# Kernel optimization log

Measured on AMD Instinct MI355X. Metric: run time of the kernel, lower is better.

The kernel has to match this reference:

```python
import jax, jax.numpy as jnp
import numpy as np

B, T, C, H = 4, 2048, 1024, 128  # batch, block_size, n_embds, head_size


def setup_inputs() -> dict:
    key = jax.random.key(0)
    k1, k2, k3, k4 = jax.random.split(key, 4)
    x = jax.random.normal(k1, (B, T, C), dtype=jnp.float32)
    # Linear(n_embds, head_size, bias=False) weights, stored as [C, H] so q = x @ Wq
    s = C ** -0.5
    Wq = jax.random.normal(k2, (C, H), dtype=jnp.float32) * s
    Wk = jax.random.normal(k3, (C, H), dtype=jnp.float32) * s
    Wv = jax.random.normal(k4, (C, H), dtype=jnp.float32) * s
    return {"x": x, "Wq": Wq, "Wk": Wk, "Wv": Wv}


def reference(x, Wq, Wk, Wv):
    # q, k, v projections (no bias)
    q = x @ Wq  # [B, T, H]
    k = x @ Wk  # [B, T, H]
    v = x @ Wv  # [B, T, H]
    scale = q.shape[-1] ** -0.5
    wei = jnp.einsum('btd,bsd->bts', q, k) * scale  # [B, T, T]
    # causal mask: positions where tril == 0 (upper triangle) get -inf
    t = wei.shape[1]
    causal = jnp.tril(jnp.ones((t, t), dtype=bool))
    wei = jnp.where(causal, wei, -jnp.inf)
    # NOTE: source uses F.softmax(wei, dim=1) -> normalize over the QUERY axis
    wei = jax.nn.softmax(wei, axis=1)
    out = wei @ v  # [B, T, H]
    return out
```

## Files before the change

### kernel.cpp

```cpp
#include <hip/hip_runtime.h>
#include <math.h>

#define B_ 4
#define T_ 2048
#define C_ 1024
#define H_ 128
#define RCHUNK 128
#define NCHUNK (T_ / RCHUNK)

typedef unsigned short u16;
typedef unsigned int   u32;
typedef short short8  __attribute__((ext_vector_type(8)));
typedef short short4v __attribute__((ext_vector_type(4)));
typedef float floatx4 __attribute__((ext_vector_type(4)));

__device__ __forceinline__ u16 f2bf(float f) {
    union { float f; u32 u; } v; v.f = f;
    return (u16)((v.u + 0x7fffu + ((v.u >> 16) & 1u)) >> 16);
}
__device__ __forceinline__ float bf2f(u16 h) {
    union { u32 u; float f; } v; v.u = ((u32)h) << 16;
    return v.f;
}

__global__ __launch_bounds__(256) void convert_x_kernel(
    const float* __restrict__ x, u16* __restrict__ xb)
{
    const size_t i = ((size_t)blockIdx.x * 256 + threadIdx.x) * 8;
    float4 a = *(const float4*)&x[i];
    float4 b = *(const float4*)&x[i + 4];
    short8 o;
    o[0]=(short)f2bf(a.x); o[1]=(short)f2bf(a.y); o[2]=(short)f2bf(a.z); o[3]=(short)f2bf(a.w);
    o[4]=(short)f2bf(b.x); o[5]=(short)f2bf(b.y); o[6]=(short)f2bf(b.z); o[7]=(short)f2bf(b.w);
    *(short8*)&xb[i] = o;
}

__global__ __launch_bounds__(256) void convert_w_kernel(
    const float* __restrict__ Wq, const float* __restrict__ Wk,
    const float* __restrict__ Wv, u16* __restrict__ Wt)
{
    const int k0 = blockIdx.x * 64, n0 = blockIdx.y * 64, widx = blockIdx.z;
    const float* W = (widx == 0) ? Wq : (widx == 1) ? Wk : Wv;

    __shared__ float ts[64][68];
    for (int i = threadIdx.x; i < 64 * 16; i += 256) {
        int r = i >> 4, c4 = i & 15;
        float4 v = *(const float4*)&W[(size_t)(k0 + r) * H_ + n0 + c4 * 4];
        ts[r][c4 * 4 + 0] = v.x; ts[r][c4 * 4 + 1] = v.y;
        ts[r][c4 * 4 + 2] = v.z; ts[r][c4 * 4 + 3] = v.w;
    }
    __syncthreads();
    for (int i = threadIdx.x; i < 64 * 16; i += 256) {
        int n = i >> 4, k4 = i & 15;
        short4v o;
        #pragma unroll
        for (int j = 0; j < 4; ++j) o[j] = (short)f2bf(ts[k4 * 4 + j][n]);
        *(short4v*)&Wt[(size_t)widx * H_ * C_ + (size_t)(n0 + n) * C_ + k0 + k4 * 4] = o;
    }
}

__global__ __launch_bounds__(256) void qkv_gemm_kernel(
    const u16* __restrict__ xb, const u16* __restrict__ Wt,
    u16* __restrict__ Qb, u16* __restrict__ Kb, u16* __restrict__ Vt)
{
    const int m0   = blockIdx.x * 64;
    const int widx = blockIdx.y;
    const u16* Wg = Wt + (size_t)widx * H_ * C_;

    __shared__ u16 As[64 * 136];
    __shared__ u16 Bs[128 * 136];

    const int w    = threadIdx.x >> 6;
    const int lane = threadIdx.x & 63;
    const int q    = lane >> 4, r = lane & 15;

    floatx4 acc[8] = {};

    for (int k0 = 0; k0 < C_; k0 += 128) {
        for (int i = threadIdx.x; i < 64 * 16; i += 256) {
            int rr = i >> 4, c = i & 15;
            *(float4*)&As[rr * 136 + c * 8] =
                *(const float4*)&xb[(size_t)(m0 + rr) * C_ + k0 + c * 8];
        }
        for (int i = threadIdx.x; i < 128 * 16; i += 256) {
            int rr = i >> 4, c = i & 15;
            *(float4*)&Bs[rr * 136 + c * 8] =
                *(const float4*)&Wg[(size_t)rr * C_ + k0 + c * 8];
        }
        __syncthreads();

        #pragma unroll
        for (int kk = 0; kk < 4; ++kk) {
            short8 af = *(const short8*)&As[(16 * w + r) * 136 + kk * 32 + q * 8];
            #pragma unroll
            for (int nt = 0; nt < 8; ++nt) {
                short8 bf = *(const short8*)&Bs[(16 * nt + r) * 136 + kk * 32 + q * 8];
                acc[nt] = __builtin_amdgcn_mfma_f32_16x16x32_bf16(af, bf, acc[nt], 0, 0, 0);
            }
        }
        __syncthreads();
    }

    if (widx == 2) {
        const int bb  = m0 / T_;
        const int tt0 = (m0 - bb * T_) + 16 * w + q * 4;
        #pragma unroll
        for (int nt = 0; nt < 8; ++nt) {
            short4v o;
            #pragma unroll
            for (int reg = 0; reg < 4; ++reg) o[reg] = (short)f2bf(acc[nt][reg]);
            *(short4v*)&Vt[((size_t)bb * H_ + 16 * nt + r) * T_ + tt0] = o;
        }
    } else {
        u16* dst = (widx == 0) ? Qb : Kb;
        #pragma unroll
        for (int nt = 0; nt < 8; ++nt)
            #pragma unroll
            for (int reg = 0; reg < 4; ++reg) {
                int mm = m0 + 16 * w + q * 4 + reg;
                int nn = 16 * nt + r;
                dst[(size_t)mm * H_ + nn] = f2bf(acc[nt][reg]);
            }
    }
}

__global__ __launch_bounds__(256) void scores_kernel(
    const u16* __restrict__ Qb, const u16* __restrict__ Kb,
    u16* __restrict__ S, float* __restrict__ pm, float* __restrict__ pl)
{
    const int si = blockIdx.x;
    const int ti = blockIdx.y;
    const int b  = blockIdx.z;
    if (si > 2 * ti + 1) return;
    const int t0 = ti * 128, s0 = si * 64;
    const bool diag = (si >= 2 * ti);

    __shared__ u16 smem[128 * 136 + 64 * 136];
    u16* Qs = smem;
    u16* Ks = smem + 128 * 136;

    const u16* Qg = Qb + ((size_t)b * T_ + t0) * H_;
    const u16* Kg = Kb + ((size_t)b * T_ + s0) * H_;

    for (int i = threadIdx.x; i < 128 * 16; i += 256) {
        int rr = i >> 4, c = i & 15;
        *(float4*)&Qs[rr * 136 + c * 8] = *(const float4*)&Qg[(size_t)rr * H_ + c * 8];
    }
    for (int i = threadIdx.x; i < 64 * 16; i += 256) {
        int rr = i >> 4, c = i & 15;
        *(float4*)&Ks[rr * 136 + c * 8] = *(const float4*)&Kg[(size_t)rr * H_ + c * 8];
    }
    __syncthreads();

    const int w    = threadIdx.x >> 6;
    const int lane = threadIdx.x & 63;
    const int q    = lane >> 4, r = lane & 15;

    floatx4 acc[2][4] = {};
    #pragma unroll
    for (int kk = 0; kk < 4; ++kk) {
        short8 a0 = *(const short8*)&Qs[(32 * w +      r) * 136 + kk * 32 + q * 8];
        short8 a1 = *(const short8*)&Qs[(32 * w + 16 + r) * 136 + kk * 32 + q * 8];
        #pragma unroll
        for (int nt = 0; nt < 4; ++nt) {
            short8 bf = *(const short8*)&Ks[(16 * nt + r) * 136 + kk * 32 + q * 8];
            acc[0][nt] = __builtin_amdgcn_mfma_f32_16x16x32_bf16(a0, bf, acc[0][nt], 0, 0, 0);
            acc[1][nt] = __builtin_amdgcn_mfma_f32_16x16x32_bf16(a1, bf, acc[1][nt], 0, 0, 0);
        }
    }
    __syncthreads();

    u16*   tile = smem;
    float* redm = (float*)(smem + 128 * 72);
    float* redl = redm + 16 * 64;

    const float scale = 0.08838834764831845f;
    #pragma unroll
    for (int nt = 0; nt < 4; ++nt) {
        const int s = s0 + 16 * nt + r;
        float mx = -INFINITY, sm = 0.f;
        #pragma unroll
        for (int mt = 0; mt < 2; ++mt)
            #pragma unroll
            for (int reg = 0; reg < 4; ++reg) {
                const int tl = 32 * w + 16 * mt + q * 4 + reg;
                const float v = acc[mt][nt][reg] * scale;
                tile[tl * 72 + 16 * nt + r] = f2bf(v);
                if (!diag || (t0 + tl) >= s) {
                    float mn = fmaxf(mx, v);
                    sm = sm * __expf(mx - mn) + __expf(v - mn);
                    mx = mn;
                }
            }
        redm[(4 * w + q) * 64 + 16 * nt + r] = mx;
        redl[(4 * w + q) * 64 + 16 * nt + r] = sm;
    }
    __syncthreads();

    if (threadIdx.x < 64) {
        const int c = threadIdx.x;
        float M = -INFINITY;
        #pragma unroll
        for (int g = 0; g < 16; ++g) M = fmaxf(M, redm[g * 64 + c]);
        float L = 0.f;
        #pragma unroll
        for (int g = 0; g < 16; ++g) {
            float lg = redl[g * 64 + c];
            if (lg > 0.f) L += lg * __expf(redm[g * 64 + c] - M);
        }
        const size_t o = ((size_t)b * NCHUNK + ti) * T_ + s0 + c;
        pm[o] = M;
        pl[o] = L;
    }

    u16* Sg = S + ((size_t)b * T_ + t0) * T_ + s0;
    for (int i = threadIdx.x; i < 128 * 8; i += 256) {
        int tl = i >> 3, c8 = i & 7;
        *(float4*)&Sg[(size_t)tl * T_ + c8 * 8] = *(float4*)&tile[tl * 72 + c8 * 8];
    }
}

__global__ __launch_bounds__(256) void stats_reduce_kernel(
    const float* __restrict__ pm, const float* __restrict__ pl,
    float* __restrict__ m, float* __restrict__ linv)
{
    const int idx = blockIdx.x * 256 + threadIdx.x;
    const int b = idx >> 11, s = idx & (T_ - 1);
    const int c0 = s >> 7;

    float M = -INFINITY;
    for (int c = c0; c < NCHUNK; ++c)
        M = fmaxf(M, pm[((size_t)b * NCHUNK + c) * T_ + s]);

    float L = 0.f;
    for (int c = c0; c < NCHUNK; ++c) {
        float mc = pm[((size_t)b * NCHUNK + c) * T_ + s];
        float lc = pl[((size_t)b * NCHUNK + c) * T_ + s];
        if (lc > 0.f) L += lc * __expf(mc - M);
    }
    m[idx]    = M;
    linv[idx] = 1.0f / L;
}

__global__ __launch_bounds__(256) void out_kernel(
    const u16* __restrict__ S, const u16* __restrict__ Vt,
    const float* __restrict__ m, const float* __restrict__ linv,
    float* __restrict__ out)
{
    const int b  = blockIdx.y;
    const int tb = (int)(gridDim.x - 1 - blockIdx.x);
    const int t0 = tb * 16;
    const int nchunks = (t0 + 79) >> 6;

    const int w    = threadIdx.x >> 6;
    const int lane = threadIdx.x & 63;
    const int q    = lane >> 4, r = lane & 15;
    const int t    = t0 + r;

    const u16*   Sb  = S    + ((size_t)b * T_ + t) * T_;
    const float* mB  = m    + (size_t)b * T_;
    const float* lB  = linv + (size_t)b * T_;
    const u16*   VtB = Vt   + (size_t)b * H_ * T_;

    floatx4 acc[8] = {};

    for (int ci = w; ci < nchunks; ci += 4) {
        const int s0 = ci * 64;
        #pragma unroll
        for (int kk = 0; kk < 2; ++kk) {
            const int sb = s0 + kk * 32 + q * 8;
            short8 sraw = *(const short8*)&Sb[sb];
            float mv[8], lv[8];
            *(float4*)&mv[0] = *(const float4*)&mB[sb];
            *(float4*)&mv[4] = *(const float4*)&mB[sb + 4];
            *(float4*)&lv[0] = *(const float4*)&lB[sb];
            *(float4*)&lv[4] = *(const float4*)&lB[sb + 4];

            short8 af;
            #pragma unroll
            for (int j = 0; j < 8; ++j) {
                float wj = 0.f;
                if (sb + j <= t)
                    wj = __expf(bf2f((u16)sraw[j]) - mv[j]) * lv[j];
                af[j] = (short)f2bf(wj);
            }
            #pragma unroll
            for (int nt = 0; nt < 8; ++nt) {
                short8 bf = *(const short8*)&VtB[(size_t)(16 * nt + r) * T_ + sb];
                acc[nt] = __builtin_amdgcn_mfma_f32_16x16x32_bf16(af, bf, acc[nt], 0, 0, 0);
            }
        }
    }

    __shared__ float red[4][16 * 128];
    #pragma unroll
    for (int nt = 0; nt < 8; ++nt)
        #pragma unroll
        for (int reg = 0; reg < 4; ++reg)
            red[w][(q * 4 + reg) * 128 + 16 * nt + r] = acc[nt][reg];
    __syncthreads();

    float* outB = out + ((size_t)b * T_ + t0) * H_;
    for (int i = threadIdx.x; i < 16 * 128; i += 256)
        outB[i] = red[0][i] + red[1][i] + red[2][i] + red[3][i];
}

extern "C" void kernel_launch(void* const* d_in, const int* in_sizes, int n_in,
                              void* d_out, int out_size, void* d_ws, size_t ws_size,
                              hipStream_t stream) {
    const float* x  = (const float*)d_in[0];
    const float* Wq = (const float*)d_in[1];
    const float* Wk = (const float*)d_in[2];
    const float* Wv = (const float*)d_in[3];
    float* out = (float*)d_out;

    u16*   S    = (u16*)d_ws;
    float* m    = (float*)(S + (size_t)B_ * T_ * T_);
    float* linv = m + (size_t)B_ * T_;
    u16*   Wt   = (u16*)(linv + (size_t)B_ * T_);
    u16*   Qb   = Wt + (size_t)3 * H_ * C_;
    u16*   Kb   = Qb + (size_t)B_ * T_ * H_;
    u16*   Vt   = Kb + (size_t)B_ * T_ * H_;
    u16*   xb   = S;

    float* pm = (float*)d_out;
    float* pl = pm + (size_t)B_ * NCHUNK * T_;

    convert_x_kernel  <<<dim3(B_ * T_ * C_ / (256 * 8)), dim3(256), 0, stream>>>(x, xb);
    convert_w_kernel  <<<dim3(C_ / 64, H_ / 64, 3),      dim3(256), 0, stream>>>(Wq, Wk, Wv, Wt);
    qkv_gemm_kernel   <<<dim3(B_ * T_ / 64, 3),          dim3(256), 0, stream>>>(xb, Wt, Qb, Kb, Vt);
    scores_kernel     <<<dim3(32, 16, B_),               dim3(256), 0, stream>>>(Qb, Kb, S, pm, pl);
    stats_reduce_kernel<<<dim3(B_ * T_ / 256),           dim3(256), 0, stream>>>(pm, pl, m, linv);
    out_kernel        <<<dim3(T_ / 16, B_),              dim3(256), 0, stream>>>(S, Vt, m, linv, out);
}
```

Measured before the change: 183.9 us.

## Recompute scores in output kernel instead of materializing S; fuse x conversion into GEMM

The scores kernel no longer writes the full bf16 score matrix to global memory and only produces per-chunk column max/sum statistics. The output kernel recomputes QK^T per 64x64 tile from Q and K in shared memory, applies the column-softmax normalisation, and multiplies by V. This avoids writing and reading the large B*T*T score matrix. Separately, the fp32-to-bf16 conversion of x moves into the QKV GEMM load path, which removes one kernel launch and an intermediate buffer. In exchange QK^T is computed twice, and the output kernel loops serially over up to 32 chunks per block with barriers, using larger tiles and fewer blocks.

```diff
diff --git a/kernel.cpp b/kernel.cpp
--- a/kernel.cpp
+++ b/kernel.cpp
@@ -18,22 +18,6 @@
     union { float f; u32 u; } v; v.f = f;
     return (u16)((v.u + 0x7fffu + ((v.u >> 16) & 1u)) >> 16);
 }
-__device__ __forceinline__ float bf2f(u16 h) {
-    union { u32 u; float f; } v; v.u = ((u32)h) << 16;
-    return v.f;
-}
-
-__global__ __launch_bounds__(256) void convert_x_kernel(
-    const float* __restrict__ x, u16* __restrict__ xb)
-{
-    const size_t i = ((size_t)blockIdx.x * 256 + threadIdx.x) * 8;
-    float4 a = *(const float4*)&x[i];
-    float4 b = *(const float4*)&x[i + 4];
-    short8 o;
-    o[0]=(short)f2bf(a.x); o[1]=(short)f2bf(a.y); o[2]=(short)f2bf(a.z); o[3]=(short)f2bf(a.w);
-    o[4]=(short)f2bf(b.x); o[5]=(short)f2bf(b.y); o[6]=(short)f2bf(b.z); o[7]=(short)f2bf(b.w);
-    *(short8*)&xb[i] = o;
-}
 
 __global__ __launch_bounds__(256) void convert_w_kernel(
     const float* __restrict__ Wq, const float* __restrict__ Wk,
@@ -60,7 +44,7 @@
 }
 
 __global__ __launch_bounds__(256) void qkv_gemm_kernel(
-    const u16* __restrict__ xb, const u16* __restrict__ Wt,
+    const float* __restrict__ x, const u16* __restrict__ Wt,
     u16* __restrict__ Qb, u16* __restrict__ Kb, u16* __restrict__ Vt)
 {
     const int m0   = blockIdx.x * 64;
@@ -79,8 +63,15 @@
     for (int k0 = 0; k0 < C_; k0 += 128) {
         for (int i = threadIdx.x; i < 64 * 16; i += 256) {
             int rr = i >> 4, c = i & 15;
-            *(float4*)&As[rr * 136 + c * 8] =
-                *(const float4*)&xb[(size_t)(m0 + rr) * C_ + k0 + c * 8];
+            const float* xg = &x[(size_t)(m0 + rr) * C_ + k0 + c * 8];
+            float4 a = *(const float4*)xg;
+            float4 b = *(const float4*)(xg + 4);
+            short8 o;
+            o[0]=(short)f2bf(a.x); o[1]=(short)f2bf(a.y);
+            o[2]=(short)f2bf(a.z); o[3]=(short)f2bf(a.w);
+            o[4]=(short)f2bf(b.x); o[5]=(short)f2bf(b.y);
+            o[6]=(short)f2bf(b.z); o[7]=(short)f2bf(b.w);
+            *(short8*)&As[rr * 136 + c * 8] = o;
         }
         for (int i = threadIdx.x; i < 128 * 16; i += 256) {
             int rr = i >> 4, c = i & 15;
@@ -124,9 +115,9 @@
     }
 }
 
-__global__ __launch_bounds__(256) void scores_kernel(
+__global__ __launch_bounds__(256) void stats_kernel(
     const u16* __restrict__ Qb, const u16* __restrict__ Kb,
-    u16* __restrict__ S, float* __restrict__ pm, float* __restrict__ pl)
+    float* __restrict__ pm, float* __restrict__ pl)
 {
     const int si = blockIdx.x;
     const int ti = blockIdx.y;
@@ -170,8 +161,7 @@
     }
     __syncthreads();
 
-    u16*   tile = smem;
-    float* redm = (float*)(smem + 128 * 72);
+    float* redm = (float*)smem;
     float* redl = redm + 16 * 64;
 
     const float scale = 0.08838834764831845f;
@@ -185,7 +175,6 @@
             for (int reg = 0; reg < 4; ++reg) {
                 const int tl = 32 * w + 16 * mt + q * 4 + reg;
                 const float v = acc[mt][nt][reg] * scale;
-                tile[tl * 72 + 16 * nt + r] = f2bf(v);
                 if (!diag || (t0 + tl) >= s) {
                     float mn = fmaxf(mx, v);
                     sm = sm * __expf(mx - mn) + __expf(v - mn);
@@ -212,12 +201,6 @@
         pm[o] = M;
         pl[o] = L;
     }
-
-    u16* Sg = S + ((size_t)b * T_ + t0) * T_ + s0;
-    for (int i = threadIdx.x; i < 128 * 8; i += 256) {
-        int tl = i >> 3, c8 = i & 7;
-        *(float4*)&Sg[(size_t)tl * T_ + c8 * 8] = *(float4*)&tile[tl * 72 + c8 * 8];
-    }
 }
 
 __global__ __launch_bounds__(256) void stats_reduce_kernel(
@@ -243,66 +226,96 @@
 }
 
 __global__ __launch_bounds__(256) void out_kernel(
-    const u16* __restrict__ S, const u16* __restrict__ Vt,
+    const u16* __restrict__ Qb, const u16* __restrict__ Kb,
+    const u16* __restrict__ Vt,
     const float* __restrict__ m, const float* __restrict__ linv,
     float* __restrict__ out)
 {
     const int b  = blockIdx.y;
     const int tb = (int)(gridDim.x - 1 - blockIdx.x);
-    const int t0 = tb * 16;
-    const int nchunks = (t0 + 79) >> 6;
+    const int t0 = tb * 64;
+    const int nch = tb + 1;
+
+    __shared__ u16 Qs[64 * 136];
+    __shared__ u16 Ks[64 * 136];
+    __shared__ u16 Ps[64 * 72];
+    __shared__ float ms[64], ls[64];
 
     const int w    = threadIdx.x >> 6;
     const int lane = threadIdx.x & 63;
     const int q    = lane >> 4, r = lane & 15;
-    const int t    = t0 + r;
-
-    const u16*   Sb  = S    + ((size_t)b * T_ + t) * T_;
+
+    const u16* Qg = Qb + ((size_t)b * T_ + t0) * H_;
+    for (int i = threadIdx.x; i < 64 * 16; i += 256) {
+        int rr = i >> 4, c = i & 15;
+        *(float4*)&Qs[rr * 136 + c * 8] = *(const float4*)&Qg[(size_t)rr * H_ + c * 8];
+    }
+
     const float* mB  = m    + (size_t)b * T_;
     const float* lB  = linv + (size_t)b * T_;
     const u16*   VtB = Vt   + (size_t)b * H_ * T_;
-
-    floatx4 acc[8] = {};
-
-    for (int ci = w; ci < nchunks; ci += 4) {
+    const float scale = 0.08838834764831845f;
+
+    floatx4 acc_o[8] = {};
+
+    for (int ci = 0; ci < nch; ++ci) {
         const int s0 = ci * 64;
-        #pragma unroll
-        for (int kk = 0; kk < 2; ++kk) {
-            const int sb = s0 + kk * 32 + q * 8;
-            short8 sraw = *(const short8*)&Sb[sb];
-            float mv[8], lv[8];
-            *(float4*)&mv[0] = *(const float4*)&mB[sb];
-            *(float4*)&mv[4] = *(const float4*)&mB[sb + 4];
-            *(float4*)&lv[0] = *(const float4*)&lB[sb];
-            *(float4*)&lv[4] = *(const float4*)&lB[sb + 4];
-
-            short8 af;
-            #pragma unroll
-            for (int j = 0; j < 8; ++j) {
-                float wj = 0.f;
-                if (sb + j <= t)
-                    wj = __expf(bf2f((u16)sraw[j]) - mv[j]) * lv[j];
-                af[j] = (short)f2bf(wj);
-            }
+        const u16* Kg = Kb + ((size_t)b * T_ + s0) * H_;
+        __syncthreads();
+        for (int i = threadIdx.x; i < 64 * 16; i += 256) {
+            int rr = i >> 4, c = i & 15;
+            *(float4*)&Ks[rr * 136 + c * 8] = *(const float4*)&Kg[(size_t)rr * H_ + c * 8];
+        }
+        if (threadIdx.x < 64) {
+            ms[threadIdx.x] = mB[s0 + threadIdx.x];
+            ls[threadIdx.x] = lB[s0 + threadIdx.x];
+        }
+        __syncthreads();
+
+        floatx4 accs[4] = {};
+        #pragma unroll
+        for (int kk = 0; kk < 4; ++kk) {
+            short8 af = *(const short8*)&Qs[(16 * w + r) * 136 + kk * 32 + q * 8];
+            #pragma unroll
+            for (int nt = 0; nt < 4; ++nt) {
+                short8 bf = *(const short8*)&Ks[(16 * nt + r) * 136 + kk * 32 + q * 8];
+                accs[nt] = __builtin_amdgcn_mfma_f32_16x16x32_bf16(af, bf, accs[nt], 0, 0, 0);
+            }
+        }
+
+        const bool last = (ci == nch - 1);
+        #pragma unroll
+        for (int nt = 0; nt < 4; ++nt) {
+            const int sl = 16 * nt + r;
+            const float mm = ms[sl];
+            const float ll = ls[sl];
+            #pragma unroll
+            for (int reg = 0; reg < 4; ++reg) {
+                const int tl = 16 * w + q * 4 + reg;
+                float p = 0.f;
+                if (!last || sl <= tl)
+                    p = __expf(accs[nt][reg] * scale - mm) * ll;
+                Ps[tl * 72 + sl] = f2bf(p);
+            }
+        }
+
+        #pragma unroll
+        for (int kk2 = 0; kk2 < 2; ++kk2) {
+            short8 af = *(const short8*)&Ps[(16 * w + r) * 72 + kk2 * 32 + q * 8];
             #pragma unroll
             for (int nt = 0; nt < 8; ++nt) {
-                short8 bf = *(const short8*)&VtB[(size_t)(16 * nt + r) * T_ + sb];
-                acc[nt] = __builtin_amdgcn_mfma_f32_16x16x32_bf16(af, bf, acc[nt], 0, 0, 0);
-            }
-        }
-    }
-
-    __shared__ float red[4][16 * 128];
+                short8 bf = *(const short8*)&VtB[(size_t)(16 * nt + r) * T_ + s0 + kk2 * 32 + q * 8];
+                acc_o[nt] = __builtin_amdgcn_mfma_f32_16x16x32_bf16(af, bf, acc_o[nt], 0, 0, 0);
+            }
+        }
+    }
+
+    float* outB = out + ((size_t)b * T_ + t0 + 16 * w) * H_;
     #pragma unroll
     for (int nt = 0; nt < 8; ++nt)
         #pragma unroll
         for (int reg = 0; reg < 4; ++reg)
-            red[w][(q * 4 + reg) * 128 + 16 * nt + r] = acc[nt][reg];
-    __syncthreads();
-
-    float* outB = out + ((size_t)b * T_ + t0) * H_;
-    for (int i = threadIdx.x; i < 16 * 128; i += 256)
-        outB[i] = red[0][i] + red[1][i] + red[2][i] + red[3][i];
+            outB[(size_t)(q * 4 + reg) * H_ + 16 * nt + r] = acc_o[nt][reg];
 }
 
 extern "C" void kernel_launch(void* const* d_in, const int* in_sizes, int n_in,
@@ -314,22 +327,19 @@
     const float* Wv = (const float*)d_in[3];
     float* out = (float*)d_out;
 
-    u16*   S    = (u16*)d_ws;
-    float* m    = (float*)(S + (size_t)B_ * T_ * T_);
+    float* m    = (float*)d_ws;
     float* linv = m + (size_t)B_ * T_;
     u16*   Wt   = (u16*)(linv + (size_t)B_ * T_);
     u16*   Qb   = Wt + (size_t)3 * H_ * C_;
     u16*   Kb   = Qb + (size_t)B_ * T_ * H_;
     u16*   Vt   = Kb + (size_t)B_ * T_ * H_;
-    u16*   xb   = S;
 
     float* pm = (float*)d_out;
     float* pl = pm + (size_t)B_ * NCHUNK * T_;
 
-    convert_x_kernel  <<<dim3(B_ * T_ * C_ / (256 * 8)), dim3(256), 0, stream>>>(x, xb);
-    convert_w_kernel  <<<dim3(C_ / 64, H_ / 64, 3),      dim3(256), 0, stream>>>(Wq, Wk, Wv, Wt);
-    qkv_gemm_kernel   <<<dim3(B_ * T_ / 64, 3),          dim3(256), 0, stream>>>(xb, Wt, Qb, Kb, Vt);
-    scores_kernel     <<<dim3(32, 16, B_),               dim3(256), 0, stream>>>(Qb, Kb, S, pm, pl);
-    stats_reduce_kernel<<<dim3(B_ * T_ / 256),           dim3(256), 0, stream>>>(pm, pl, m, linv);
-    out_kernel        <<<dim3(T_ / 16, B_),              dim3(256), 0, stream>>>(S, Vt, m, linv, out);
-}
+    convert_w_kernel  <<<dim3(C_ / 64, H_ / 64, 3),    dim3(256), 0, stream>>>(Wq, Wk, Wv, Wt);
+    qkv_gemm_kernel   <<<dim3(B_ * T_ / 64, 3),        dim3(256), 0, stream>>>(x, Wt, Qb, Kb, Vt);
+    stats_kernel      <<<dim3(32, 16, B_),             dim3(256), 0, stream>>>(Qb, Kb, pm, pl);
+    stats_reduce_kernel<<<dim3(B_ * T_ / 256),         dim3(256), 0, stream>>>(pm, pl, m, linv);
+    out_kernel        <<<dim3(T_ / 64, B_),            dim3(256), 0, stream>>>(Qb, Kb, Vt, m, linv, out);
+}
```

After: 272.6 us. 1.48x slower.

## Fuse x bf16 conversion into QKV GEMM and prefetch S chunks in out kernel

Applied to the files above, without the earlier changes.

Drops the separate x-to-bf16 conversion kernel. The QKV GEMM now reads fp32 x directly and converts each tile as it loads it into shared memory, which removes one launch and a full write and read of the bf16 copy of x. In exchange, x is re-read in fp32 once for each of the three weight matrices. The out kernel also software-pipelines its loads, fetching the next chunk's scores and softmax stats into registers while the current chunk is computed. This hides global-load latency at the cost of more registers.

```diff
diff --git a/kernel.cpp b/kernel.cpp
--- a/kernel.cpp
+++ b/kernel.cpp
@@ -23,18 +23,6 @@
     return v.f;
 }
 
-__global__ __launch_bounds__(256) void convert_x_kernel(
-    const float* __restrict__ x, u16* __restrict__ xb)
-{
-    const size_t i = ((size_t)blockIdx.x * 256 + threadIdx.x) * 8;
-    float4 a = *(const float4*)&x[i];
-    float4 b = *(const float4*)&x[i + 4];
-    short8 o;
-    o[0]=(short)f2bf(a.x); o[1]=(short)f2bf(a.y); o[2]=(short)f2bf(a.z); o[3]=(short)f2bf(a.w);
-    o[4]=(short)f2bf(b.x); o[5]=(short)f2bf(b.y); o[6]=(short)f2bf(b.z); o[7]=(short)f2bf(b.w);
-    *(short8*)&xb[i] = o;
-}
-
 __global__ __launch_bounds__(256) void convert_w_kernel(
     const float* __restrict__ Wq, const float* __restrict__ Wk,
     const float* __restrict__ Wv, u16* __restrict__ Wt)
@@ -60,7 +48,7 @@
 }
 
 __global__ __launch_bounds__(256) void qkv_gemm_kernel(
-    const u16* __restrict__ xb, const u16* __restrict__ Wt,
+    const float* __restrict__ x, const u16* __restrict__ Wt,
     u16* __restrict__ Qb, u16* __restrict__ Kb, u16* __restrict__ Vt)
 {
     const int m0   = blockIdx.x * 64;
@@ -79,8 +67,15 @@
     for (int k0 = 0; k0 < C_; k0 += 128) {
         for (int i = threadIdx.x; i < 64 * 16; i += 256) {
             int rr = i >> 4, c = i & 15;
-            *(float4*)&As[rr * 136 + c * 8] =
-                *(const float4*)&xb[(size_t)(m0 + rr) * C_ + k0 + c * 8];
+            const float* xg = &x[(size_t)(m0 + rr) * C_ + k0 + c * 8];
+            float4 a = *(const float4*)xg;
+            float4 b = *(const float4*)(xg + 4);
+            short8 o;
+            o[0]=(short)f2bf(a.x); o[1]=(short)f2bf(a.y);
+            o[2]=(short)f2bf(a.z); o[3]=(short)f2bf(a.w);
+            o[4]=(short)f2bf(b.x); o[5]=(short)f2bf(b.y);
+            o[6]=(short)f2bf(b.z); o[7]=(short)f2bf(b.w);
+            *(short8*)&As[rr * 136 + c * 8] = o;
         }
         for (int i = threadIdx.x; i < 128 * 16; i += 256) {
             int rr = i >> 4, c = i & 15;
@@ -264,24 +259,53 @@
 
     floatx4 acc[8] = {};
 
-    for (int ci = w; ci < nchunks; ci += 4) {
+    short8 sc[2];  float4 mc[2][2], lc[2][2];
+
+    int ci = w;
+    if (ci < nchunks) {
         const int s0 = ci * 64;
         #pragma unroll
         for (int kk = 0; kk < 2; ++kk) {
             const int sb = s0 + kk * 32 + q * 8;
-            short8 sraw = *(const short8*)&Sb[sb];
+            sc[kk]    = *(const short8*)&Sb[sb];
+            mc[kk][0] = *(const float4*)&mB[sb];
+            mc[kk][1] = *(const float4*)&mB[sb + 4];
+            lc[kk][0] = *(const float4*)&lB[sb];
+            lc[kk][1] = *(const float4*)&lB[sb + 4];
+        }
+    }
+
+    while (ci < nchunks) {
+        const int s0 = ci * 64;
+        const int cn = ci + 4;
+
+        short8 sn[2];  float4 mn[2][2], ln[2][2];
+        if (cn < nchunks) {
+            const int s0n = cn * 64;
+            #pragma unroll
+            for (int kk = 0; kk < 2; ++kk) {
+                const int sb = s0n + kk * 32 + q * 8;
+                sn[kk]    = *(const short8*)&Sb[sb];
+                mn[kk][0] = *(const float4*)&mB[sb];
+                mn[kk][1] = *(const float4*)&mB[sb + 4];
+                ln[kk][0] = *(const float4*)&lB[sb];
+                ln[kk][1] = *(const float4*)&lB[sb + 4];
+            }
+        }
+
+        #pragma unroll
+        for (int kk = 0; kk < 2; ++kk) {
+            const int sb = s0 + kk * 32 + q * 8;
             float mv[8], lv[8];
-            *(float4*)&mv[0] = *(const float4*)&mB[sb];
-            *(float4*)&mv[4] = *(const float4*)&mB[sb + 4];
-            *(float4*)&lv[0] = *(const float4*)&lB[sb];
-            *(float4*)&lv[4] = *(const float4*)&lB[sb + 4];
+            *(float4*)&mv[0] = mc[kk][0];  *(float4*)&mv[4] = mc[kk][1];
+            *(float4*)&lv[0] = lc[kk][0];  *(float4*)&lv[4] = lc[kk][1];
 
             short8 af;
             #pragma unroll
             for (int j = 0; j < 8; ++j) {
                 float wj = 0.f;
                 if (sb + j <= t)
-                    wj = __expf(bf2f((u16)sraw[j]) - mv[j]) * lv[j];
+                    wj = __expf(bf2f((u16)sc[kk][j]) - mv[j]) * lv[j];
                 af[j] = (short)f2bf(wj);
             }
             #pragma unroll
@@ -290,6 +314,14 @@
                 acc[nt] = __builtin_amdgcn_mfma_f32_16x16x32_bf16(af, bf, acc[nt], 0, 0, 0);
             }
         }
+
+        #pragma unroll
+        for (int kk = 0; kk < 2; ++kk) {
+            sc[kk] = sn[kk];
+            mc[kk][0] = mn[kk][0];  mc[kk][1] = mn[kk][1];
+            lc[kk][0] = ln[kk][0];  lc[kk][1] = ln[kk][1];
+        }
+        ci = cn;
     }
 
     __shared__ float red[4][16 * 128];
@@ -321,15 +353,13 @@
     u16*   Qb   = Wt + (size_t)3 * H_ * C_;
     u16*   Kb   = Qb + (size_t)B_ * T_ * H_;
     u16*   Vt   = Kb + (size_t)B_ * T_ * H_;
-    u16*   xb   = S;
 
     float* pm = (float*)d_out;
     float* pl = pm + (size_t)B_ * NCHUNK * T_;
 
-    convert_x_kernel  <<<dim3(B_ * T_ * C_ / (256 * 8)), dim3(256), 0, stream>>>(x, xb);
-    convert_w_kernel  <<<dim3(C_ / 64, H_ / 64, 3),      dim3(256), 0, stream>>>(Wq, Wk, Wv, Wt);
-    qkv_gemm_kernel   <<<dim3(B_ * T_ / 64, 3),          dim3(256), 0, stream>>>(xb, Wt, Qb, Kb, Vt);
-    scores_kernel     <<<dim3(32, 16, B_),               dim3(256), 0, stream>>>(Qb, Kb, S, pm, pl);
-    stats_reduce_kernel<<<dim3(B_ * T_ / 256),           dim3(256), 0, stream>>>(pm, pl, m, linv);
-    out_kernel        <<<dim3(T_ / 16, B_),              dim3(256), 0, stream>>>(S, Vt, m, linv, out);
-}
+    convert_w_kernel  <<<dim3(C_ / 64, H_ / 64, 3),    dim3(256), 0, stream>>>(Wq, Wk, Wv, Wt);
+    qkv_gemm_kernel   <<<dim3(B_ * T_ / 64, 3),        dim3(256), 0, stream>>>(x, Wt, Qb, Kb, Vt);
+    scores_kernel     <<<dim3(32, 16, B_),             dim3(256), 0, stream>>>(Qb, Kb, S, pm, pl);
+    stats_reduce_kernel<<<dim3(B_ * T_ / 256),         dim3(256), 0, stream>>>(pm, pl, m, linv);
+    out_kernel        <<<dim3(T_ / 16, B_),            dim3(256), 0, stream>>>(S, Vt, m, linv, out);
+}
```

Measured after the change: 177.2 us. 3.6% less time.
